# Kernel tuning notes

Hardware: AMD Instinct MI355X
Metric: run time of the kernel (lower is better)

The kernel has to match this reference:

```python
import jax, jax.numpy as jnp
import numpy as np

N, E, D, H, DH, FF, C, L = 50000, 640000, 128, 8, 16, 256, 5, 6
EPS = 1e-5


def _bn(x, g, b):
    # training-mode BatchNorm1d over the node dimension
    m = jnp.mean(x, axis=0)
    v = jnp.var(x, axis=0)
    return (x - m) * jax.lax.rsqrt(v + EPS) * g + b


def _sparse_mha(x, src, dst, Wq, Wk, Wv, Wo):
    # edge-restricted multi-head attention: softmax over incoming edges per dst node
    q = (x @ Wq).reshape(N, H, DH)
    k = (x @ Wk).reshape(N, H, DH)
    v = (x @ Wv).reshape(N, H, DH)
    s = jnp.einsum('ehd,ehd->eh', q[dst], k[src]) * (1.0 / np.sqrt(DH))  # [E,H]
    smax = jax.ops.segment_max(s, dst, num_segments=N)
    smax = jnp.where(jnp.isfinite(smax), smax, 0.0)  # guard isolated nodes
    e = jnp.exp(s - smax[dst])
    den = jax.ops.segment_sum(e, dst, num_segments=N)
    alpha = e / jnp.where(den > 0, den, 1.0)[dst]
    out = jax.ops.segment_sum(alpha[:, :, None] * v[src], dst, num_segments=N)  # [N,H,DH]
    return out.reshape(N, D) @ Wo


def setup_inputs() -> dict:
    key = jax.random.key(0)
    ks = jax.random.split(key, 18)
    f = lambda k, shp, sc: (jax.random.normal(k, shp, jnp.float32) * sc)
    return {
        'x': jax.random.normal(ks[0], (N, D), jnp.float32),
        'edge_index': jax.random.randint(ks[1], (2, E), 0, N),
        'Wq': f(ks[2], (L, D, D), 0.08),
        'Wk': f(ks[3], (L, D, D), 0.08),
        'Wv': f(ks[4], (L, D, D), 0.08),
        'Wo': f(ks[5], (L, D, D), 0.08),
        'g1': jnp.ones((L, D), jnp.float32),
        'bn1': jnp.zeros((L, D), jnp.float32),
        'W1': f(ks[6], (L, D, FF), 0.08),
        'bf1': jnp.zeros((L, FF), jnp.float32),
        'W2': f(ks[7], (L, FF, D), 0.06),
        'bf2': jnp.zeros((L, D), jnp.float32),
        'g2': jnp.ones((L, D), jnp.float32),
        'bn2': jnp.zeros((L, D), jnp.float32),
        'Wp': f(ks[8], (D, C), 0.08),
        'bp': jnp.zeros((C,), jnp.float32),
    }


def reference(x, edge_index, Wq, Wk, Wv, Wo, g1, bn1, W1, bf1, W2, bf2, g2, bn2, Wp, bp):
    src, dst = edge_index[0], edge_index[1]
    for i in range(L):  # fixed small layer count
        res = x  # residual is Identity (num_input == num_output)
        a = _sparse_mha(x, src, dst, Wq[i], Wk[i], Wv[i], Wo[i])
        x = _bn(a + res, g1[i], bn1[i])
        h = jax.nn.relu(x @ W1[i] + bf1[i])  # leakiness=0 -> relu
        x = _bn(x + (h @ W2[i] + bf2[i]), g2[i], bn2[i])
    node_pred = x @ Wp + bp
    return node_pred
```

## Files before the change

### kernel.cpp

```cpp
#include <hip/hip_runtime.h>
#include <hip/hip_bf16.h>
#include <cstdio>

#define NN 50000
#define EE 640000
#define DD 128
#define HH 8
#define DH 16
#define FFD 256
#define CC 5
#define LL 6
#define EPSV 1e-5f
#define HPAD 264

typedef __attribute__((ext_vector_type(8))) short bf16x8;
typedef __attribute__((ext_vector_type(8))) unsigned short ushort8;
typedef __attribute__((ext_vector_type(4))) float f32x4;

__device__ __forceinline__ float bfu2f(unsigned short u) {
  union { unsigned int i; float f; } x; x.i = ((unsigned int)u) << 16; return x.f;
}
__device__ __forceinline__ unsigned short f2bf(float f) {
  union { float f; unsigned int i; } x; x.f = f;
  unsigned int r = (x.i + 0x7fffu + ((x.i >> 16) & 1u)) >> 16;
  return (unsigned short)r;
}

__global__ void detect_kernel(const unsigned int* __restrict__ g1w, int* __restrict__ flag) {
  if (threadIdx.x == 0 && blockIdx.x == 0) *flag = (g1w[0] == 0x3F803F80u) ? 1 : 0;
}

struct ConvJobs { const void* in[8]; float* out[8]; int n[8]; };
__global__ __launch_bounds__(256) void convert_batch_kernel(ConvJobs jobs, const int* __restrict__ flag) {
  int b = blockIdx.x;
  const void* in = jobs.in[b];
  float* out = jobs.out[b];
  int n = jobs.n[b];
  int use_bf = *flag;
  for (int i = threadIdx.x; i < n; i += 256) {
    if (use_bf) out[i] = bfu2f(((const unsigned short*)in)[i]);
    else        out[i] = ((const float*)in)[i];
  }
}

__global__ __launch_bounds__(256) void to_bf16_kernel(const void* __restrict__ in,
                                                      unsigned short* __restrict__ out, int n,
                                                      const int* __restrict__ flag) {
  int i = blockIdx.x * blockDim.x + threadIdx.x;
  if (i >= n) return;
  if (*flag) out[i] = ((const unsigned short*)in)[i];
  else       out[i] = f2bf(((const float*)in)[i]);
}

__global__ __launch_bounds__(256) void t_qkv_tiled(const void* __restrict__ wq, const void* __restrict__ wk,
                                                   const void* __restrict__ wv,
                                                   unsigned short* __restrict__ qkvT,
                                                   const int* __restrict__ flag) {
  __shared__ unsigned short tile[32][33];
  int l = blockIdx.z / 3, which = blockIdx.z % 3;
  const void* in = (which == 0) ? wq : (which == 1) ? wk : wv;
  size_t off = (size_t)l * DD * DD;
  unsigned short* out = qkvT + (size_t)l * 384 * DD + (size_t)which * DD * DD;
  int tx = threadIdx.x & 31, ty = threadIdx.x >> 5;
  int k0 = blockIdx.x * 32, n0 = blockIdx.y * 32;
  int use_bf = *flag;
#pragma unroll
  for (int i = 0; i < 4; i++) {
    int k = k0 + ty + i * 8;
    unsigned short v;
    if (use_bf) v = ((const unsigned short*)in)[off + (size_t)k * DD + n0 + tx];
    else        v = f2bf(((const float*)in)[off + (size_t)k * DD + n0 + tx]);
    tile[ty + i * 8][tx] = v;
  }
  __syncthreads();
#pragma unroll
  for (int i = 0; i < 4; i++) {
    int n = n0 + ty + i * 8;
    out[(size_t)n * DD + k0 + tx] = tile[tx][ty + i * 8];
  }
}

__global__ __launch_bounds__(256) void t_w_tiled(const void* __restrict__ in,
                                                 unsigned short* __restrict__ out,
                                                 int K, int N, const int* __restrict__ flag) {
  __shared__ unsigned short tile[32][33];
  int l = blockIdx.z;
  size_t off = (size_t)l * K * N;
  unsigned short* o = out + (size_t)l * K * N;
  int tx = threadIdx.x & 31, ty = threadIdx.x >> 5;
  int k0 = blockIdx.x * 32, n0 = blockIdx.y * 32;
  int use_bf = *flag;
#pragma unroll
  for (int i = 0; i < 4; i++) {
    int k = k0 + ty + i * 8;
    unsigned short v;
    if (use_bf) v = ((const unsigned short*)in)[off + (size_t)k * N + n0 + tx];
    else        v = f2bf(((const float*)in)[off + (size_t)k * N + n0 + tx]);
    tile[ty + i * 8][tx] = v;
  }
  __syncthreads();
#pragma unroll
  for (int i = 0; i < 4; i++) {
    int n = n0 + ty + i * 8;
    o[(size_t)n * K + k0 + tx] = tile[tx][ty + i * 8];
  }
}

__global__ __launch_bounds__(256) void zero_kernel(int* __restrict__ p, int n) {
  int i = blockIdx.x * blockDim.x + threadIdx.x;
  if (i < n) p[i] = 0;
}

__global__ void init_id_kernel(float* __restrict__ stats_id, float* __restrict__ g_id, float* __restrict__ b_id) {
  int t = threadIdx.x;
  if (t < 128) {
    stats_id[t] = 0.f;
    stats_id[128 + t] = (float)NN * (1.0f - EPSV);
    g_id[t] = 1.f;
    b_id[t] = 0.f;
  }
}

__global__ __launch_bounds__(256) void count_kernel(const int* __restrict__ dst, int* __restrict__ counts) {
  int e = blockIdx.x * blockDim.x + threadIdx.x;
  if (e < EE) atomicAdd(&counts[dst[e]], 1);
}

__global__ __launch_bounds__(256) void scan1_kernel(const int* __restrict__ counts,
                                                    int* __restrict__ row_ptr, int* __restrict__ partials) {
  __shared__ int sh[256];
  int t = threadIdx.x;
  int i = blockIdx.x * 256 + t;
  int v = (i < NN) ? counts[i] : 0;
  sh[t] = v; __syncthreads();
#pragma unroll
  for (int off = 1; off < 256; off <<= 1) {
    int u = (t >= off) ? sh[t - off] : 0;
    __syncthreads();
    sh[t] += u;
    __syncthreads();
  }
  if (i < NN) row_ptr[i] = sh[t] - v;
  if (t == 255) partials[blockIdx.x] = sh[t];
}

__global__ __launch_bounds__(256) void scan2_kernel(int* __restrict__ partials, int nb) {
  __shared__ int sh[256];
  int t = threadIdx.x;
  int v = (t < nb) ? partials[t] : 0;
  sh[t] = v; __syncthreads();
#pragma unroll
  for (int off = 1; off < 256; off <<= 1) {
    int u = (t >= off) ? sh[t - off] : 0;
    __syncthreads();
    sh[t] += u;
    __syncthreads();
  }
  if (t < nb) partials[t] = sh[t] - v;
}

__global__ __launch_bounds__(256) void scan3_kernel(int* __restrict__ row_ptr, const int* __restrict__ partials) {
  int i = blockIdx.x * 256 + threadIdx.x;
  if (i < NN) row_ptr[i] += partials[blockIdx.x];
  if (i == 0) row_ptr[NN] = EE;
}

__global__ __launch_bounds__(256) void fill_kernel(const int* __restrict__ src, const int* __restrict__ dst,
                                                   const int* __restrict__ row_ptr, int* __restrict__ cursor,
                                                   int* __restrict__ csr_src) {
  int e = blockIdx.x * blockDim.x + threadIdx.x;
  if (e < EE) {
    int d = dst[e];
    int pos = row_ptr[d] + atomicAdd(&cursor[d], 1);
    csr_src[pos] = src[e];
  }
}

__global__ __launch_bounds__(128) void fold_kernel(const float* __restrict__ stats,
                                                   const float* __restrict__ g,
                                                   const float* __restrict__ b,
                                                   const unsigned short* __restrict__ WT,
                                                   const float* __restrict__ base_bias,
                                                   unsigned short* __restrict__ WTo,
                                                   float* __restrict__ bias_o,
                                                   float* __restrict__ ss_o) {
  __shared__ float ssc[128];
  __shared__ float ssh[128];
  __shared__ float part[2];
  int t = threadIdx.x;
  float mean = stats[t] * (1.f / NN);
  float var  = fmaxf(stats[128 + t] * (1.f / NN) - mean * mean, 0.f);
  float sc = g[t] * rsqrtf(var + EPSV);
  float sh = b[t] - mean * sc;
  ssc[t] = sc; ssh[t] = sh;
  if (blockIdx.x == 0) { ss_o[t] = sc; ss_o[128 + t] = sh; }
  __syncthreads();
  int c = blockIdx.x;
  float w = bfu2f(WT[(size_t)c * 128 + t]);
  WTo[(size_t)c * 128 + t] = f2bf(ssc[t] * w);
  float contrib = ssh[t] * w;
#pragma unroll
  for (int off = 32; off; off >>= 1) contrib += __shfl_down(contrib, off);
  if ((t & 63) == 0) part[t >> 6] = contrib;
  __syncthreads();
  if (t == 0) bias_o[c] = (base_bias ? base_bias[c] : 0.f) + part[0] + part[1];
}

template<int K, bool RELU, bool HASBIAS, bool RESAFF, bool STATS>
__global__ __launch_bounds__(256) void mfma_gemm(const unsigned short* __restrict__ A,
                                                 const unsigned short* __restrict__ BT,
                                                 const float* __restrict__ bias,
                                                 const unsigned short* __restrict__ resid,
                                                 const float* __restrict__ rss,
                                                 unsigned short* __restrict__ C,
                                                 float* __restrict__ stats,
                                                 int M, int ldc) {
  __shared__ float lsum[64];
  __shared__ float lsq[64];
  int tid = threadIdx.x;
  int lane = tid & 63, wave = tid >> 6;
  int m0 = blockIdx.x * 128 + wave * 32;
  int n0 = blockIdx.y * 64;
  int lm = lane & 15;
  int quad = lane >> 4;
  int kq = quad * 8;

  int rowA[2];
#pragma unroll
  for (int r = 0; r < 2; r++) {
    int rr = m0 + 16 * r + lm;
    rowA[r] = (rr < M) ? rr : (M - 1);
  }
  const unsigned short* aptr0 = A + (size_t)rowA[0] * K + kq;
  const unsigned short* aptr1 = A + (size_t)rowA[1] * K + kq;
  const unsigned short* bptr[4];
#pragma unroll
  for (int c = 0; c < 4; c++)
    bptr[c] = BT + (size_t)(n0 + 16 * c + lm) * K + kq;

  f32x4 acc[2][4];
#pragma unroll
  for (int r = 0; r < 2; r++)
#pragma unroll
    for (int c = 0; c < 4; c++) acc[r][c] = (f32x4){0.f, 0.f, 0.f, 0.f};

#pragma unroll
  for (int kc = 0; kc < K; kc += 128) {
    bf16x8 a[2][4], b[4][4];
#pragma unroll
    for (int ks = 0; ks < 4; ks++) {
      a[0][ks] = *(const bf16x8*)(aptr0 + kc + ks * 32);
      a[1][ks] = *(const bf16x8*)(aptr1 + kc + ks * 32);
    }
#pragma unroll
    for (int c = 0; c < 4; c++)
#pragma unroll
      for (int ks = 0; ks < 4; ks++)
        b[c][ks] = *(const bf16x8*)(bptr[c] + kc + ks * 32);
#pragma unroll
    for (int ks = 0; ks < 4; ks++)
#pragma unroll
      for (int r = 0; r < 2; r++)
#pragma unroll
        for (int c = 0; c < 4; c++)
          acc[r][c] = __builtin_amdgcn_mfma_f32_16x16x32_bf16(b[c][ks], a[r][ks], acc[r][c], 0, 0, 0);
  }

  if (STATS) {
    if (tid < 64) { lsum[tid] = 0.f; lsq[tid] = 0.f; }
    __syncthreads();
  }

  float st_s[4][4], st_q[4][4];
  if (STATS) {
#pragma unroll
    for (int c = 0; c < 4; c++)
#pragma unroll
      for (int reg = 0; reg < 4; reg++) { st_s[c][reg] = 0.f; st_q[c][reg] = 0.f; }
  }

#pragma unroll
  for (int r = 0; r < 2; r++) {
    int row = m0 + 16 * r + lm;
    if (row >= M) continue;
#pragma unroll
    for (int c = 0; c < 4; c++) {
      int col = n0 + 16 * c + quad * 4;
      float4 bv = HASBIAS ? *(const float4*)(bias + col) : make_float4(0.f, 0.f, 0.f, 0.f);
      float o[4];
      o[0] = acc[r][c][0] + bv.x; o[1] = acc[r][c][1] + bv.y;
      o[2] = acc[r][c][2] + bv.z; o[3] = acc[r][c][3] + bv.w;
      if (RESAFF) {
        ushort4 rr = *(const ushort4*)(resid + (size_t)row * ldc + col);
        float4 rsc = *(const float4*)(rss + col);
        float4 rsh = *(const float4*)(rss + 128 + col);
        o[0] += bfu2f(rr.x) * rsc.x + rsh.x;
        o[1] += bfu2f(rr.y) * rsc.y + rsh.y;
        o[2] += bfu2f(rr.z) * rsc.z + rsh.z;
        o[3] += bfu2f(rr.w) * rsc.w + rsh.w;
      }
      if (RELU) {
        o[0] = fmaxf(o[0], 0.f); o[1] = fmaxf(o[1], 0.f);
        o[2] = fmaxf(o[2], 0.f); o[3] = fmaxf(o[3], 0.f);
      }
      size_t idx = (size_t)row * ldc + col;
      ushort4 w;
      w.x = f2bf(o[0]); w.y = f2bf(o[1]); w.z = f2bf(o[2]); w.w = f2bf(o[3]);
      *(ushort4*)(C + idx) = w;
      if (STATS) {
#pragma unroll
        for (int reg = 0; reg < 4; reg++) {
          st_s[c][reg] += o[reg];
          st_q[c][reg] = fmaf(o[reg], o[reg], st_q[c][reg]);
        }
      }
    }
  }

  if (STATS) {
#pragma unroll
    for (int c = 0; c < 4; c++)
#pragma unroll
      for (int reg = 0; reg < 4; reg++) {
        float s = st_s[c][reg], q = st_q[c][reg];
        s += __shfl_xor(s, 1);  q += __shfl_xor(q, 1);
        s += __shfl_xor(s, 2);  q += __shfl_xor(q, 2);
        s += __shfl_xor(s, 4);  q += __shfl_xor(q, 4);
        s += __shfl_xor(s, 8);  q += __shfl_xor(q, 8);
        if (lm == 0) {
          atomicAdd(&lsum[16 * c + quad * 4 + reg], s);
          atomicAdd(&lsq[16 * c + quad * 4 + reg], q);
        }
      }
    __syncthreads();
    if (tid < 64) {
      atomicAdd(&stats[n0 + tid], lsum[tid]);
      atomicAdd(&stats[128 + n0 + tid], lsq[tid]);
    }
  }
}

__global__ __launch_bounds__(256) void ffn_fused(const unsigned short* __restrict__ A,
                                                 const unsigned short* __restrict__ W1T,
                                                 const float* __restrict__ b1,
                                                 const unsigned short* __restrict__ W2T,
                                                 const float* __restrict__ b2,
                                                 const float* __restrict__ rss,
                                                 unsigned short* __restrict__ C,
                                                 float* __restrict__ stats, int M) {
  __shared__ unsigned short hl[128 * HPAD];
  __shared__ float lsum[128];
  __shared__ float lsq[128];
  int tid = threadIdx.x;
  int lane = tid & 63, wave = tid >> 6;
  int m0 = blockIdx.x * 128 + wave * 32;
  int lm = lane & 15, quad = lane >> 4, kq = quad * 8;

  if (tid < 128) { lsum[tid] = 0.f; lsq[tid] = 0.f; }
  __syncthreads();

  int rowA[2];
#pragma unroll
  for (int r = 0; r < 2; r++) {
    int rr = m0 + 16 * r + lm;
    rowA[r] = (rr < M) ? rr : (M - 1);
  }
  bf16x8 a[2][4];
#pragma unroll
  for (int ks = 0; ks < 4; ks++) {
    a[0][ks] = *(const bf16x8*)(A + (size_t)rowA[0] * 128 + ks * 32 + kq);
    a[1][ks] = *(const bf16x8*)(A + (size_t)rowA[1] * 128 + ks * 32 + kq);
  }

#pragma unroll
  for (int nt = 0; nt < 4; nt++) {
    int n0 = nt * 64;
    bf16x8 b[4][4];
#pragma unroll
    for (int c = 0; c < 4; c++)
#pragma unroll
      for (int ks = 0; ks < 4; ks++)
        b[c][ks] = *(const bf16x8*)(W1T + (size_t)(n0 + 16 * c + lm) * 128 + ks * 32 + kq);
    f32x4 acc[2][4];
#pragma unroll
    for (int r = 0; r < 2; r++)
#pragma unroll
      for (int c = 0; c < 4; c++) acc[r][c] = (f32x4){0.f, 0.f, 0.f, 0.f};
#pragma unroll
    for (int ks = 0; ks < 4; ks++)
#pragma unroll
      for (int r = 0; r < 2; r++)
#pragma unroll
        for (int c = 0; c < 4; c++)
          acc[r][c] = __builtin_amdgcn_mfma_f32_16x16x32_bf16(b[c][ks], a[r][ks], acc[r][c], 0, 0, 0);
#pragma unroll
    for (int r = 0; r < 2; r++) {
      int lrow = wave * 32 + 16 * r + lm;
#pragma unroll
      for (int c = 0; c < 4; c++) {
        int col = n0 + 16 * c + quad * 4;
        float4 bv = *(const float4*)(b1 + col);
        ushort4 w;
        w.x = f2bf(fmaxf(acc[r][c][0] + bv.x, 0.f));
        w.y = f2bf(fmaxf(acc[r][c][1] + bv.y, 0.f));
        w.z = f2bf(fmaxf(acc[r][c][2] + bv.z, 0.f));
        w.w = f2bf(fmaxf(acc[r][c][3] + bv.w, 0.f));
        *(ushort4*)(hl + (size_t)lrow * HPAD + col) = w;
      }
    }
  }

#pragma unroll
  for (int nt = 0; nt < 2; nt++) {
    int n0 = nt * 64;
    f32x4 acc[2][4];
#pragma unroll
    for (int r = 0; r < 2; r++)
#pragma unroll
      for (int c = 0; c < 4; c++) acc[r][c] = (f32x4){0.f, 0.f, 0.f, 0.f};
#pragma unroll
    for (int kc = 0; kc < 256; kc += 128) {
      bf16x8 ha[2][4], b[4][4];
#pragma unroll
      for (int ks = 0; ks < 4; ks++) {
        ha[0][ks] = *(const bf16x8*)(hl + (size_t)(wave * 32 + lm) * HPAD + kc + ks * 32 + kq);
        ha[1][ks] = *(const bf16x8*)(hl + (size_t)(wave * 32 + 16 + lm) * HPAD + kc + ks * 32 + kq);
      }
#pragma unroll
      for (int c = 0; c < 4; c++)
#pragma unroll
        for (int ks = 0; ks < 4; ks++)
          b[c][ks] = *(const bf16x8*)(W2T + (size_t)(n0 + 16 * c + lm) * 256 + kc + ks * 32 + kq);
#pragma unroll
      for (int ks = 0; ks < 4; ks++)
#pragma unroll
        for (int r = 0; r < 2; r++)
#pragma unroll
          for (int c = 0; c < 4; c++)
            acc[r][c] = __builtin_amdgcn_mfma_f32_16x16x32_bf16(b[c][ks], ha[r][ks], acc[r][c], 0, 0, 0);
    }

    float st_s[4][4], st_q[4][4];
#pragma unroll
    for (int c = 0; c < 4; c++)
#pragma unroll
      for (int reg = 0; reg < 4; reg++) { st_s[c][reg] = 0.f; st_q[c][reg] = 0.f; }

#pragma unroll
    for (int r = 0; r < 2; r++) {
      int row = m0 + 16 * r + lm;
      if (row >= M) continue;
#pragma unroll
      for (int c = 0; c < 4; c++) {
        int col = n0 + 16 * c + quad * 4;
        float4 bv = *(const float4*)(b2 + col);
        float o[4];
        o[0] = acc[r][c][0] + bv.x; o[1] = acc[r][c][1] + bv.y;
        o[2] = acc[r][c][2] + bv.z; o[3] = acc[r][c][3] + bv.w;
        ushort4 rr = *(const ushort4*)(A + (size_t)row * 128 + col);
        float4 rsc = *(const float4*)(rss + col);
        float4 rsh = *(const float4*)(rss + 128 + col);
        o[0] += bfu2f(rr.x) * rsc.x + rsh.x;
        o[1] += bfu2f(rr.y) * rsc.y + rsh.y;
        o[2] += bfu2f(rr.z) * rsc.z + rsh.z;
        o[3] += bfu2f(rr.w) * rsc.w + rsh.w;
        ushort4 w;
        w.x = f2bf(o[0]); w.y = f2bf(o[1]); w.z = f2bf(o[2]); w.w = f2bf(o[3]);
        *(ushort4*)(C + (size_t)row * 128 + col) = w;
#pragma unroll
        for (int reg = 0; reg < 4; reg++) {
          st_s[c][reg] += o[reg];
          st_q[c][reg] = fmaf(o[reg], o[reg], st_q[c][reg]);
        }
      }
    }
#pragma unroll
    for (int c = 0; c < 4; c++)
#pragma unroll
      for (int reg = 0; reg < 4; reg++) {
        float s = st_s[c][reg], q = st_q[c][reg];
        s += __shfl_xor(s, 1);  q += __shfl_xor(q, 1);
        s += __shfl_xor(s, 2);  q += __shfl_xor(q, 2);
        s += __shfl_xor(s, 4);  q += __shfl_xor(q, 4);
        s += __shfl_xor(s, 8);  q += __shfl_xor(q, 8);
        if (lm == 0) {
          atomicAdd(&lsum[n0 + 16 * c + quad * 4 + reg], s);
          atomicAdd(&lsq[n0 + 16 * c + quad * 4 + reg], q);
        }
      }
  }
  __syncthreads();
  if (tid < 128) {
    atomicAdd(&stats[tid], lsum[tid]);
    atomicAdd(&stats[128 + tid], lsq[tid]);
  }
}

__global__ __launch_bounds__(256) void attn_kernel(const unsigned short* __restrict__ qkv,
                                                   const int* __restrict__ row_ptr,
                                                   const int* __restrict__ csr_src,
                                                   unsigned short* __restrict__ t1) {
  int t = blockIdx.x * blockDim.x + threadIdx.x;
  int half = t & 1;
  int nh = t >> 1;
  int n = nh >> 3, h = nh & 7;
  const unsigned short* qp = qkv + (size_t)n * 384 + h * 16 + half * 8;
  float qf[8];
  {
    bf16x8 q0 = *(const bf16x8*)qp;
#pragma unroll
    for (int i = 0; i < 8; i++) qf[i] = bfu2f((unsigned short)q0[i]);
  }
  float m = -3.0e38f, l = 0.f;
  float A[8];
#pragma unroll
  for (int i = 0; i < 8; i++) A[i] = 0.f;
  int e0 = row_ptr[n], e1 = row_ptr[n + 1];
  if (e0 < e1) {
    int last = e1 - 1;
    const size_t hoff = 128 + (size_t)h * 16 + half * 8;
    int s0 = csr_src[e0];
    const unsigned short* kp0 = qkv + (size_t)s0 * 384 + hoff;
    bf16x8 ck = *(const bf16x8*)kp0;
    bf16x8 cv = *(const bf16x8*)(kp0 + 128);
    int ei1 = (e0 + 1 <= last) ? e0 + 1 : last;
    int s1 = csr_src[ei1];
    const unsigned short* kp1 = qkv + (size_t)s1 * 384 + hoff;
    bf16x8 nk = *(const bf16x8*)kp1;
    bf16x8 nv = *(const bf16x8*)(kp1 + 128);
    for (int e = e0; e < e1; e++) {
      int e2 = (e + 2 <= last) ? e + 2 : last;
      int s2 = csr_src[e2];
      const unsigned short* kp2 = qkv + (size_t)s2 * 384 + hoff;
      bf16x8 k2 = *(const bf16x8*)kp2;
      bf16x8 v2 = *(const bf16x8*)(kp2 + 128);

      float part = 0.f;
#pragma unroll
      for (int i = 0; i < 8; i++) part += qf[i] * bfu2f((unsigned short)ck[i]);
      float sc = (part + __shfl_xor(part, 1)) * 0.25f;
      float mn = fmaxf(m, sc);
      float cf = __expf(m - mn);
      float p  = __expf(sc - mn);
      l = l * cf + p;
#pragma unroll
      for (int i = 0; i < 8; i++)
        A[i] = A[i] * cf + p * bfu2f((unsigned short)cv[i]);
      m = mn;
      ck = nk; cv = nv; nk = k2; nv = v2;
    }
  }
  float inv = (l > 0.f) ? 1.f / l : 0.f;
  ushort8 o0;
#pragma unroll
  for (int i = 0; i < 8; i++) o0[i] = f2bf(A[i] * inv);
  unsigned short* op = t1 + (size_t)n * 128 + h * 16 + half * 8;
  *(ushort8*)op = o0;
}

__global__ __launch_bounds__(256) void proj_kernel(const unsigned short* __restrict__ y2,
                                                   const float* __restrict__ statsL,
                                                   const float* __restrict__ g,
                                                   const float* __restrict__ b,
                                                   const float* __restrict__ Wp,
                                                   const float* __restrict__ bp,
                                                   void* __restrict__ out,
                                                   const int* __restrict__ flag) {
  __shared__ float W[DD * CC];
  __shared__ float bias[CC];
  __shared__ float ssc[128];
  __shared__ float ssh[128];
  int t = threadIdx.x;
  for (int i = t; i < DD * CC; i += 256) W[i] = Wp[i];
  if (t < CC) bias[t] = bp[t];
  if (t < 128) {
    float mean = statsL[t] * (1.f / NN);
    float var  = fmaxf(statsL[128 + t] * (1.f / NN) - mean * mean, 0.f);
    float sc = g[t] * rsqrtf(var + EPSV);
    ssc[t] = sc;
    ssh[t] = b[t] - mean * sc;
  }
  __syncthreads();
  int n = blockIdx.x * 256 + t;
  if (n >= NN) return;
  float acc[CC];
#pragma unroll
  for (int c = 0; c < CC; c++) acc[c] = bias[c];
  const ushort4* xp = (const ushort4*)(y2 + (size_t)n * DD);
#pragma unroll
  for (int k4 = 0; k4 < DD / 4; k4++) {
    ushort4 u = xp[k4];
    int k = k4 * 4;
    float a0 = bfu2f(u.x) * ssc[k + 0] + ssh[k + 0];
    float a1 = bfu2f(u.y) * ssc[k + 1] + ssh[k + 1];
    float a2 = bfu2f(u.z) * ssc[k + 2] + ssh[k + 2];
    float a3 = bfu2f(u.w) * ssc[k + 3] + ssh[k + 3];
    const float* w = &W[k * CC];
#pragma unroll
    for (int c = 0; c < CC; c++)
      acc[c] += a0 * w[c] + a1 * w[CC + c] + a2 * w[2 * CC + c] + a3 * w[3 * CC + c];
  }
  if (*flag) {
    __hip_bfloat16* o16 = (__hip_bfloat16*)out;
#pragma unroll
    for (int c = 0; c < CC; c++) o16[(size_t)n * CC + c] = __float2bfloat16(acc[c]);
  } else {
    float* o32 = (float*)out;
#pragma unroll
    for (int c = 0; c < CC; c++) o32[(size_t)n * CC + c] = acc[c];
  }
}

extern "C" void kernel_launch(void* const* d_in, const int* in_sizes, int n_in,
                              void* d_out, int out_size, void* d_ws, size_t ws_size,
                              hipStream_t stream) {
  const int* ei = (const int*)d_in[1];

  char* p = (char*)d_ws;
  auto carve = [&](size_t bytes) { char* r = p; p += (bytes + 255) & ~(size_t)255; return (void*)r; };
  unsigned short* xb   = (unsigned short*)carve((size_t)NN * DD * 2);
  unsigned short* qkv  = (unsigned short*)carve((size_t)NN * 384 * 2);
  unsigned short* t1   = (unsigned short*)carve((size_t)NN * DD * 2);
  unsigned short* y1   = (unsigned short*)carve((size_t)NN * DD * 2);
  unsigned short* y2   = (unsigned short*)carve((size_t)NN * DD * 2);
  float* stats  = (float*)carve(12 * 256 * 4);
  float* stats_id = (float*)carve(256 * 4);
  float* ss     = (float*)carve(12 * 256 * 4);
  float* ss_id  = (float*)carve(256 * 4);
  float* g_id   = (float*)carve(128 * 4);
  float* b_id   = (float*)carve(128 * 4);
  int* row_ptr = (int*)carve((size_t)(NN + 1) * 4);
  int* cursor  = (int*)carve((size_t)NN * 4);
  int* counts  = (int*)carve((size_t)NN * 4);
  int* csr_src = (int*)carve((size_t)EE * 4);
  int* flag    = (int*)carve(256);
  int* partials = (int*)carve(256 * 4);
  unsigned short* qkvT = (unsigned short*)carve((size_t)LL * 384 * DD * 2);
  unsigned short* WoT  = (unsigned short*)carve((size_t)LL * DD * DD * 2);
  unsigned short* W1T  = (unsigned short*)carve((size_t)LL * FFD * DD * 2);
  unsigned short* W2T  = (unsigned short*)carve((size_t)LL * DD * FFD * 2);
  unsigned short* qkvTf = (unsigned short*)carve((size_t)384 * DD * 2);
  unsigned short* W1Tf  = (unsigned short*)carve((size_t)FFD * DD * 2);
  float* qkv_bias = (float*)carve(384 * 4);
  float* w1_bias  = (float*)carve(256 * 4);
  float* g1_f  = (float*)carve((size_t)LL * DD * 4);
  float* bn1_f = (float*)carve((size_t)LL * DD * 4);
  float* bf1_f = (float*)carve((size_t)LL * FFD * 4);
  float* bf2_f = (float*)carve((size_t)LL * DD * 4);
  float* g2_f  = (float*)carve((size_t)LL * DD * 4);
  float* bn2_f = (float*)carve((size_t)LL * DD * 4);
  float* Wp_f  = (float*)carve((size_t)DD * CC * 4);
  float* bp_f  = (float*)carve((size_t)CC * 4);
  size_t need = (size_t)(p - (char*)d_ws);
  if (need > ws_size) {
    fprintf(stderr, "kernel_launch: workspace too small: need %zu, have %zu\n", need, ws_size);
    return;
  }

  const int* src  = ei;
  const int* dstp = ei + EE;

  detect_kernel<<<1, 64, 0, stream>>>((const unsigned int*)d_in[6], flag);
  to_bf16_kernel<<<(NN * DD + 255) / 256, 256, 0, stream>>>(d_in[0], xb, NN * DD, flag);

  {
    ConvJobs j;
    j.in[0] = d_in[6];  j.out[0] = g1_f;  j.n[0] = LL * DD;
    j.in[1] = d_in[7];  j.out[1] = bn1_f; j.n[1] = LL * DD;
    j.in[2] = d_in[9];  j.out[2] = bf1_f; j.n[2] = LL * FFD;
    j.in[3] = d_in[11]; j.out[3] = bf2_f; j.n[3] = LL * DD;
    j.in[4] = d_in[12]; j.out[4] = g2_f;  j.n[4] = LL * DD;
    j.in[5] = d_in[13]; j.out[5] = bn2_f; j.n[5] = LL * DD;
    j.in[6] = d_in[14]; j.out[6] = Wp_f;  j.n[6] = DD * CC;
    j.in[7] = d_in[15]; j.out[7] = bp_f;  j.n[7] = CC;
    convert_batch_kernel<<<8, 256, 0, stream>>>(j, flag);
  }

  t_qkv_tiled<<<dim3(4, 4, 3 * LL), 256, 0, stream>>>(d_in[2], d_in[3], d_in[4], qkvT, flag);
  t_w_tiled<<<dim3(4, 4, LL), 256, 0, stream>>>(d_in[5], WoT, DD, DD, flag);
  t_w_tiled<<<dim3(4, 8, LL), 256, 0, stream>>>(d_in[8], W1T, DD, FFD, flag);
  t_w_tiled<<<dim3(8, 4, LL), 256, 0, stream>>>(d_in[10], W2T, FFD, DD, flag);

  zero_kernel<<<12, 256, 0, stream>>>((int*)stats, 12 * 256);
  init_id_kernel<<<1, 128, 0, stream>>>(stats_id, g_id, b_id);
  zero_kernel<<<(NN + 255) / 256, 256, 0, stream>>>(counts, NN);
  zero_kernel<<<(NN + 255) / 256, 256, 0, stream>>>(cursor, NN);

  const int NB = (NN + 255) / 256;
  count_kernel<<<(EE + 255) / 256, 256, 0, stream>>>(dstp, counts);
  scan1_kernel<<<NB, 256, 0, stream>>>(counts, row_ptr, partials);
  scan2_kernel<<<1, 256, 0, stream>>>(partials, NB);
  scan3_kernel<<<NB, 256, 0, stream>>>(row_ptr, partials);
  fill_kernel<<<(EE + 255) / 256, 256, 0, stream>>>(src, dstp, row_ptr, cursor, csr_src);

  const int gm = (NN + 127) / 128;
  for (int layer = 0; layer < LL; layer++) {
    const unsigned short* WoT_l = WoT + (size_t)layer * DD * DD;
    const unsigned short* W1T_l = W1T + (size_t)layer * FFD * DD;
    const unsigned short* W2T_l = W2T + (size_t)layer * DD * FFD;
    float* st1 = stats + (size_t)(layer * 2 + 0) * 256;
    float* st2 = stats + (size_t)(layer * 2 + 1) * 256;
    float* ss1 = ss + (size_t)(layer * 2 + 0) * 256;

    const unsigned short* Ain = layer ? y2 : xb;
    const float* stats_prev = layer ? (stats + (size_t)((layer - 1) * 2 + 1) * 256) : stats_id;
    const float* g_prev = layer ? (g2_f + (size_t)(layer - 1) * DD) : g_id;
    const float* b_prev = layer ? (bn2_f + (size_t)(layer - 1) * DD) : b_id;
    float* ss_prev = layer ? (ss + (size_t)((layer - 1) * 2 + 1) * 256) : ss_id;

    fold_kernel<<<384, 128, 0, stream>>>(stats_prev, g_prev, b_prev,
                                         qkvT + (size_t)layer * 384 * DD, nullptr,
                                         qkvTf, qkv_bias, ss_prev);
    mfma_gemm<128, false, true, false, false><<<dim3(gm, 6), 256, 0, stream>>>(
        Ain, qkvTf, qkv_bias, nullptr, nullptr, qkv, nullptr, NN, 384);
    attn_kernel<<<NN * HH * 2 / 256, 256, 0, stream>>>(qkv, row_ptr, csr_src, t1);
    mfma_gemm<128, false, false, true, true><<<dim3(gm, 2), 256, 0, stream>>>(
        t1, WoT_l, nullptr, Ain, ss_prev, y1, st1, NN, 128);
    fold_kernel<<<256, 128, 0, stream>>>(st1, g1_f + (size_t)layer * DD, bn1_f + (size_t)layer * DD,
                                         W1T_l, bf1_f + (size_t)layer * FFD,
                                         W1Tf, w1_bias, ss1);
    ffn_fused<<<gm, 256, 0, stream>>>(y1, W1Tf, w1_bias, W2T_l,
                                      bf2_f + (size_t)layer * DD, ss1, y2, st2, NN);
  }

  proj_kernel<<<(NN + 255) / 256, 256, 0, stream>>>(
      y2, stats + (size_t)((LL - 1) * 2 + 1) * 256, g2_f + (size_t)(LL - 1) * DD,
      bn2_f + (size_t)(LL - 1) * DD, Wp_f, bp_f, d_out, flag);
}
```

Measured before the change: 1.248 ms.

## Split each node's edge loop across four wavefront slots with online-softmax merge

The attention kernel now gives each node a full 64-lane wavefront: four slots of 16 lanes each walk every fourth incoming edge, keeping their own running max, sum and accumulator, and are merged at the end with xor-shuffle log-sum-exp combines. This shortens the serial per-node edge chain and exposes more independent gathers in flight, aiming to hide gather latency. The cost is four times as many threads, extra exp and shuffle work for the merge, and idle slots on low-degree nodes. The explicit two-deep software prefetch is replaced by a one-ahead prefetch per slot.

```diff
diff --git a/kernel.cpp b/kernel.cpp
--- a/kernel.cpp
+++ b/kernel.cpp
@@ -500,10 +500,12 @@
                                                    const int* __restrict__ row_ptr,
                                                    const int* __restrict__ csr_src,
                                                    unsigned short* __restrict__ t1) {
-  int t = blockIdx.x * blockDim.x + threadIdx.x;
-  int half = t & 1;
-  int nh = t >> 1;
-  int n = nh >> 3, h = nh & 7;
+  int t = blockIdx.x * 256 + threadIdx.x;
+  int n = t >> 6;
+  int lane = t & 63;
+  int slot = lane >> 4;
+  int sub = lane & 15;
+  int h = sub >> 1, half = sub & 1;
   const unsigned short* qp = qkv + (size_t)n * 384 + h * 16 + half * 8;
   float qf[8];
   {
@@ -516,46 +518,58 @@
 #pragma unroll
   for (int i = 0; i < 8; i++) A[i] = 0.f;
   int e0 = row_ptr[n], e1 = row_ptr[n + 1];
+  const size_t hoff = 128 + (size_t)h * 16 + half * 8;
   if (e0 < e1) {
-    int last = e1 - 1;
-    const size_t hoff = 128 + (size_t)h * 16 + half * 8;
-    int s0 = csr_src[e0];
-    const unsigned short* kp0 = qkv + (size_t)s0 * 384 + hoff;
-    bf16x8 ck = *(const bf16x8*)kp0;
-    bf16x8 cv = *(const bf16x8*)(kp0 + 128);
-    int ei1 = (e0 + 1 <= last) ? e0 + 1 : last;
-    int s1 = csr_src[ei1];
-    const unsigned short* kp1 = qkv + (size_t)s1 * 384 + hoff;
-    bf16x8 nk = *(const bf16x8*)kp1;
-    bf16x8 nv = *(const bf16x8*)(kp1 + 128);
-    for (int e = e0; e < e1; e++) {
-      int e2 = (e + 2 <= last) ? e + 2 : last;
-      int s2 = csr_src[e2];
-      const unsigned short* kp2 = qkv + (size_t)s2 * 384 + hoff;
-      bf16x8 k2 = *(const bf16x8*)kp2;
-      bf16x8 v2 = *(const bf16x8*)(kp2 + 128);
+    int ei = e0 + slot;
+    int sv = csr_src[(ei < e1) ? ei : (e1 - 1)];
+    const unsigned short* kp = qkv + (size_t)sv * 384 + hoff;
+    bf16x8 ck = *(const bf16x8*)kp;
+    bf16x8 cv = *(const bf16x8*)(kp + 128);
+    bool cvalid = ei < e1;
+    for (int base = e0; base < e1; base += 4) {
+      int nei = base + 4 + slot;
+      int ns = csr_src[(nei < e1) ? nei : (e1 - 1)];
+      const unsigned short* np = qkv + (size_t)ns * 384 + hoff;
+      bf16x8 nk = *(const bf16x8*)np;
+      bf16x8 nv = *(const bf16x8*)(np + 128);
 
       float part = 0.f;
 #pragma unroll
       for (int i = 0; i < 8; i++) part += qf[i] * bfu2f((unsigned short)ck[i]);
       float sc = (part + __shfl_xor(part, 1)) * 0.25f;
-      float mn = fmaxf(m, sc);
+      float mn = cvalid ? fmaxf(m, sc) : m;
       float cf = __expf(m - mn);
-      float p  = __expf(sc - mn);
-      l = l * cf + p;
+      float pp = cvalid ? __expf(sc - mn) : 0.f;
+      l = l * cf + pp;
 #pragma unroll
       for (int i = 0; i < 8; i++)
-        A[i] = A[i] * cf + p * bfu2f((unsigned short)cv[i]);
+        A[i] = A[i] * cf + pp * bfu2f((unsigned short)cv[i]);
       m = mn;
-      ck = nk; cv = nv; nk = k2; nv = v2;
+      ck = nk; cv = nv; cvalid = nei < e1;
     }
   }
-  float inv = (l > 0.f) ? 1.f / l : 0.f;
-  ushort8 o0;
-#pragma unroll
-  for (int i = 0; i < 8; i++) o0[i] = f2bf(A[i] * inv);
-  unsigned short* op = t1 + (size_t)n * 128 + h * 16 + half * 8;
-  *(ushort8*)op = o0;
+#pragma unroll
+  for (int off = 16; off <= 32; off <<= 1) {
+    float mo = __shfl_xor(m, off);
+    float lo = __shfl_xor(l, off);
+    float mn = fmaxf(m, mo);
+    float a = __expf(m - mn);
+    float b = __expf(mo - mn);
+#pragma unroll
+    for (int i = 0; i < 8; i++) {
+      float Ao = __shfl_xor(A[i], off);
+      A[i] = A[i] * a + Ao * b;
+    }
+    l = l * a + lo * b;
+    m = mn;
+  }
+  if (lane < 16) {
+    float inv = (l > 0.f) ? 1.f / l : 0.f;
+    ushort8 o0;
+#pragma unroll
+    for (int i = 0; i < 8; i++) o0[i] = f2bf(A[i] * inv);
+    *(ushort8*)(t1 + (size_t)n * 128 + h * 16 + half * 8) = o0;
+  }
 }
 
 __global__ __launch_bounds__(256) void proj_kernel(const unsigned short* __restrict__ y2,
@@ -713,7 +727,7 @@
                                          qkvTf, qkv_bias, ss_prev);
     mfma_gemm<128, false, true, false, false><<<dim3(gm, 6), 256, 0, stream>>>(
         Ain, qkvTf, qkv_bias, nullptr, nullptr, qkv, nullptr, NN, 384);
-    attn_kernel<<<NN * HH * 2 / 256, 256, 0, stream>>>(qkv, row_ptr, csr_src, t1);
+    attn_kernel<<<NN * 64 / 256, 256, 0, stream>>>(qkv, row_ptr, csr_src, t1);
     mfma_gemm<128, false, false, true, true><<<dim3(gm, 2), 256, 0, stream>>>(
         t1, WoT_l, nullptr, Ain, ss_prev, y1, st1, NN, 128);
     fold_kernel<<<256, 128, 0, stream>>>(st1, g1_f + (size_t)layer * DD, bn1_f + (size_t)layer * DD,
```

After: 1.228 ms. Within noise of the previous version (-1.6%).
